# Kernel optimization log

Measured on AMD Instinct MI355X. Metric: run time of the kernel, lower is better.

The kernel has to match this reference:

```python
import jax, jax.numpy as jnp
import numpy as np
from jax import lax

SPATIAL = 4
DN = ('NCHW', 'OIHW', 'NCHW')

def setup_inputs() -> dict:
    key = jax.random.key(0)
    ks = jax.random.split(key, 6)
    b, c_in, h, w = 32, 256, 56, 56
    c_out, kk, n_exp, red = 256, 3, 3, 16
    fan = c_in * kk * kk
    return {
        'x': jax.random.normal(ks[0], (b, c_in, h, w), jnp.float32),
        'w_expert': jax.random.normal(ks[1], (n_exp, c_out, c_in, kk, kk), jnp.float32) / np.sqrt(fan),
        'route_conv_w': jax.random.normal(ks[2], (red, c_in), jnp.float32) / np.sqrt(c_in),
        'route_conv_b': jax.random.normal(ks[3], (red,), jnp.float32) * 0.05,
        'fc_w': jax.random.normal(ks[4], (n_exp, red * SPATIAL * SPATIAL), jnp.float32) / np.sqrt(red * SPATIAL * SPATIAL),
        'fc_b': jax.random.normal(ks[5], (n_exp,), jnp.float32) * 0.05,
    }

def _routing(x, route_conv_w, route_conv_b, fc_w, fc_b):
    b, c, h, w = x.shape
    # AdaptiveAvgPool2d(4): h, w divisible by 4 -> exact block mean
    pooled = x.reshape(b, c, SPATIAL, h // SPATIAL, SPATIAL, w // SPATIAL).mean(axis=(3, 5))  # [b,c,4,4]
    r = jnp.einsum('bcij,rc->brij', pooled, route_conv_w) + route_conv_b[None, :, None, None]
    r = jax.nn.relu(r).reshape(b, -1)                         # [b, red*16]
    r = jax.nn.relu(r @ fc_w.T + fc_b)                        # [b, n_exp]
    return jax.nn.sigmoid(r)

def reference(x, w_expert, route_conv_w, route_conv_b, fc_w, fc_b):
    rw = _routing(x, route_conv_w, route_conv_b, fc_w, fc_b)              # [b,k]
    cw = jnp.einsum('bk,koihw->boihw', rw, w_expert)                      # per-sample mixed weights
    def conv1(xi, wi):
        return lax.conv_general_dilated(xi[None], wi, window_strides=(1, 1),
                                        padding=[(1, 1), (1, 1)],
                                        dimension_numbers=DN)[0]
    return jax.vmap(conv1)(x, cw)  # [b, c_out, h, w]
```

## Files before the change

kernel.cpp:

```cpp
#include <hip/hip_runtime.h>
#include <hip/hip_bf16.h>
#include <stdint.h>

#define NB   32
#define CIN  256
#define COUT 256
#define WW   56
#define HW   3136
#define NEXP 3
#define KTOT 2304
#define XP   58
#define XPP  3364
#define NKT  36

typedef __attribute__((ext_vector_type(8))) __bf16 bf16x8;
typedef __attribute__((ext_vector_type(4))) float  f32x4;

#define OFF_RW     0
#define OFF_POOLED 1024
#define OFF_CWT    (1024 + 32*256*16*4)
#define CWT_BYTES  ((size_t)NB*COUT*KTOT*2)
#define OFF_XPAD   (OFF_CWT + CWT_BYTES)

#define PRE_XPAD 6272
#define PRE_POOL 8192
#define PRE_NBLK (PRE_XPAD + PRE_POOL + NB)

__global__ __launch_bounds__(256) void k_pre(const float* __restrict__ x,
                                             float* __restrict__ pooled,
                                             __bf16* __restrict__ xpad) {
    __shared__ __align__(16) char smem[8448];
    int blk = blockIdx.x;
    int t = threadIdx.x;

    if (blk < PRE_XPAD) {
        int pt = blk % 49;
        int r2 = blk / 49;
        int ct = r2 & 3;
        int b  = r2 >> 2;
        __bf16 (*lds)[66] = (__bf16(*)[66])smem;
        int pl = t & 63;
        int cb = t >> 6;
        const float* xb = x + ((size_t)(b * CIN + ct * 64)) * HW + pt * 64;
        #pragma unroll
        for (int ic = 0; ic < 16; ++ic) {
            int cl = ic * 4 + cb;
            lds[cl][pl] = (__bf16)xb[(size_t)cl * HW + pl];
        }
        __syncthreads();
        #pragma unroll
        for (int iw = 0; iw < 2; ++iw) {
            int idx = iw * 256 + t;
            int p_l = idx >> 3, c8 = (idx & 7) * 8;
            int p = pt * 64 + p_l;
            int y = p / WW, xx = p - y * WW;
            union { __bf16 h[8]; uint4 u; } pk;
            #pragma unroll
            for (int j = 0; j < 8; ++j) pk.h[j] = lds[c8 + j][p_l];
            __bf16* dst = xpad + ((size_t)b * XPP + (y + 1) * XP + (xx + 1)) * CIN
                          + ct * 64 + c8;
            *(uint4*)dst = pk.u;
        }
    } else if (blk < PRE_XPAD + PRE_POOL) {
        int j = blk - PRE_XPAD;
        int b = j >> 8, c = j & 255;
        float (*lds)[56] = (float(*)[56])smem;
        const float* xb = x + ((size_t)(b * CIN + c)) * HW;
        if (t < 224) {
            int xc = t % 56, yg = t / 56;
            const float* p = xb + (yg * 14) * WW + xc;
            float s = 0.f;
            #pragma unroll
            for (int r = 0; r < 14; ++r) s += p[r * WW];
            lds[yg][xc] = s;
        }
        __syncthreads();
        if (t < 16) {
            int sy = t >> 2, sx = t & 3;
            float s = 0.f;
            #pragma unroll
            for (int jj = 0; jj < 14; ++jj) s += lds[sy][sx * 14 + jj];
            pooled[(((size_t)b * CIN + c) << 4) + t] = s * (1.f / 196.f);
        }
    } else {
        int b = blk - (PRE_XPAD + PRE_POOL);
        for (int idx = t; idx < 228 * 32; idx += 256) {
            int pos = idx >> 5;
            int co = (idx & 31) * 8;
            int yy, xx;
            if (pos < 58)       { yy = 0;          xx = pos; }
            else if (pos < 116) { yy = 57;         xx = pos - 58; }
            else if (pos < 172) { yy = pos - 115;  xx = 0; }
            else                { yy = pos - 171;  xx = 57; }
            uint4 z = {0u, 0u, 0u, 0u};
            *(uint4*)(xpad + ((size_t)b * XPP + yy * XP + xx) * CIN + co) = z;
        }
    }
}

__global__ __launch_bounds__(256) void k_route(const float* __restrict__ pooled,
                                               const float* __restrict__ rcw,
                                               const float* __restrict__ rcb,
                                               const float* __restrict__ fcw,
                                               const float* __restrict__ fcb,
                                               float* __restrict__ rw) {
    int b = blockIdx.x;
    int t = threadIdx.x;
    int r = t >> 4, ij = t & 15;
    __shared__ float rbuf[256];
    const float* pb = pooled + (size_t)b * CIN * 16;
    float acc = rcb[r];
    for (int c = 0; c < CIN; ++c)
        acc += pb[c * 16 + ij] * rcw[r * CIN + c];
    rbuf[t] = fmaxf(acc, 0.f);
    __syncthreads();
    if (t < NEXP) {
        float a = fcb[t];
        for (int f = 0; f < 256; ++f) a += rbuf[f] * fcw[t * 256 + f];
        a = fmaxf(a, 0.f);
        rw[b * NEXP + t] = 1.f / (1.f + expf(-a));
    }
}

__global__ __launch_bounds__(256) void k_mixw(const float* __restrict__ we,
                                              const float* __restrict__ rw,
                                              __bf16* __restrict__ cwt) {
    int o = blockIdx.x;
    int i = threadIdx.x;
    float wv[3][9];
    #pragma unroll
    for (int e = 0; e < 3; ++e) {
        const float* p = we + (((size_t)e * COUT + o) * CIN + i) * 9;
        #pragma unroll
        for (int k = 0; k < 9; ++k) wv[e][k] = p[k];
    }
    for (int b = 0; b < NB; ++b) {
        float r0 = rw[b * 3 + 0], r1 = rw[b * 3 + 1], r2 = rw[b * 3 + 2];
        __bf16* op = cwt + ((size_t)(b * COUT + o)) * KTOT + i;
        #pragma unroll
        for (int k = 0; k < 9; ++k) {
            float v = r0 * wv[0][k] + r1 * wv[1][k] + r2 * wv[2][k];
            op[k * 256] = (__bf16)v;
        }
    }
}

#define GL16(g, l) __builtin_amdgcn_global_load_lds( \
    (const __attribute__((address_space(1))) uint32_t*)(g), \
    (__attribute__((address_space(3))) uint32_t*)(l), 16, 0, 0)

#define STAGE_A(o, kh, aoffn) do { \
    GL16(gA0 + (aoffn) + (kh)*64, LDS + (o)*32768 + (kh)*16384 + wid*1024); \
    GL16(gA1 + (aoffn) + (kh)*64, LDS + (o)*32768 + (kh)*16384 + 8192 + wid*1024); \
  } while (0)
#define STAGE_B(o, kh, boffn) do { \
    GL16(gB0 + (boffn) + (kh)*64, LDS + 65536 + (o)*32768 + (kh)*16384 + wid*1024); \
    GL16(gB1 + (boffn) + (kh)*64, LDS + 65536 + (o)*32768 + (kh)*16384 + 8192 + wid*1024); \
  } while (0)

#define BARRIER() do { \
    __builtin_amdgcn_sched_barrier(0); \
    __builtin_amdgcn_s_barrier(); \
    __builtin_amdgcn_sched_barrier(0); \
  } while (0)
#define VMCNT(n) do { \
    asm volatile("s_waitcnt vmcnt(" #n ")" ::: "memory"); \
    __builtin_amdgcn_sched_barrier(0); \
  } while (0)
#define LGKM0() do { \
    asm volatile("s_waitcnt lgkmcnt(0)" ::: "memory"); \
    __builtin_amdgcn_sched_barrier(0); \
  } while (0)

#define LOADF(F, base, kh, q) do { \
    F[0] = *(const bf16x8*)((base) + (kh)*16384 + (q)*4096 + 0); \
    F[1] = *(const bf16x8*)((base) + (kh)*16384 + (q)*4096 + 1024); \
    F[2] = *(const bf16x8*)((base) + (kh)*16384 + (q)*4096 + 2048); \
    F[3] = *(const bf16x8*)((base) + (kh)*16384 + (q)*4096 + 3072); \
  } while (0)
#define MM(qb, F) do { \
    _Pragma("unroll") \
    for (int mf = 0; mf < 4; ++mf) \
      _Pragma("unroll") \
      for (int nf = 0; nf < 4; ++nf) \
        acc[(qb) + mf][nf] = __builtin_amdgcn_mfma_f32_16x16x32_bf16( \
            F[mf], bq[nf], acc[(qb) + mf][nf], 0, 0, 0); \
  } while (0)

#define HALF(c, o, kh, aoffn, boffn) do { \
    VMCNT(4); \
    BARRIER(); \
    STAGE_A(o, kh, aoffn); \
    STAGE_B(o, kh, boffn); \
    { const char* aCur = LDS + (c) * 32768 + aRd; \
      const char* bCur = LDS + 65536 + (c) * 32768 + bRd; \
      LOADF(af, aCur, kh, 0); \
      LOADF(bq, bCur, kh, 0); \
      LOADF(ag, aCur, kh, 1); } \
    LGKM0(); \
    __builtin_amdgcn_s_setprio(1); \
    MM(0, af); \
    MM(4, ag); \
    __builtin_amdgcn_s_setprio(0); \
  } while (0)

__global__ __launch_bounds__(512, 2) void k_conv(const __bf16* __restrict__ cwt,
                                                 const __bf16* __restrict__ xpad,
                                                 float* __restrict__ out) {
    extern __shared__ __align__(16) char LDS[];

    int flat = blockIdx.x;
    int logical = (flat & 7) * 52 + (flat >> 3);
    int b  = logical / 13;
    int nt = logical - b * 13;

    int tid = threadIdx.x;
    int ln  = tid & 63;
    int wid = tid >> 6;
    int wr  = wid >> 2;
    int wc  = wid & 3;
    int fr  = ln & 15;
    int kw  = ln >> 4;
    int xsw = ((fr >> 1) & 3) << 4;

    const char *gA0, *gA1, *gB0, *gB1;
    {
        const char* cwb = (const char*)(cwt + (size_t)b * COUT * KTOT);
        const char* xpb = (const char*)(xpad + (size_t)b * XPP * CIN);
        #pragma unroll
        for (int i = 0; i < 2; ++i) {
            int L = i * 8192 + wid * 1024 + ln * 16;
            int U = L ^ (((L >> 7) & 3) << 4);
            int rowU = U >> 6;
            int kbU  = U & 63;
            const char* ga = cwb + (size_t)rowU * (KTOT * 2) + kbU;
            int p = nt * 256 + rowU; if (p > HW - 1) p = HW - 1;
            int y = p / WW, x = p - y * WW;
            const char* gb = xpb + (size_t)(y * XP + x) * (CIN * 2) + kbU;
            if (i == 0) { gA0 = ga; gB0 = gb; } else { gA1 = ga; gB1 = gb; }
        }
    }

    int aRd = (wr * 128 + fr) * 64 + ((kw * 16) ^ xsw);
    int bRd = (wc * 64 + fr) * 64 + ((kw * 16) ^ xsw);

    f32x4 acc[8][4];
    #pragma unroll
    for (int i = 0; i < 8; ++i)
        #pragma unroll
        for (int j = 0; j < 4; ++j)
            acc[i][j] = (f32x4){0.f, 0.f, 0.f, 0.f};

    bf16x8 af[4], ag[4], bq[4];

    STAGE_A(0, 0, 0);
    STAGE_B(0, 0, 0);
    STAGE_A(0, 1, 0);
    STAGE_B(0, 1, 0);

    for (int kt = 0; kt < NKT - 1; ++kt) {
        int c = kt & 1, o = c ^ 1;
        int ktn  = kt + 1;
        int aoffn = ktn * 128;
        int ktap = ktn >> 2;
        int kyn  = (ktap * 11) >> 5;
        int kxn  = ktap - kyn * 3;
        int boffn = (kyn * XP + kxn) * 512 + (ktn & 3) * 128;

        HALF(c, o, 0, aoffn, boffn);
        HALF(c, o, 1, aoffn, boffn);
    }

    {
        VMCNT(0);
        BARRIER();
        const char* aCur = LDS + 32768 + aRd;
        const char* bCur = LDS + 65536 + 32768 + bRd;
        LOADF(af, aCur, 0, 0); LOADF(bq, bCur, 0, 0); LOADF(ag, aCur, 0, 1);
        LGKM0();
        __builtin_amdgcn_s_setprio(1); MM(0, af); MM(4, ag);
        __builtin_amdgcn_s_setprio(0);
        LOADF(af, aCur, 1, 0); LOADF(bq, bCur, 1, 0); LOADF(ag, aCur, 1, 1);
        LGKM0();
        __builtin_amdgcn_s_setprio(1); MM(0, af); MM(4, ag);
        __builtin_amdgcn_s_setprio(0);
    }

    float* ob = out + ((size_t)(b * COUT + wr * 128)) * HW;
    int colbase = nt * 256 + wc * 64;
    int rb = (ln >> 4) * 4;
    #pragma unroll
    for (int q = 0; q < 2; ++q)
        #pragma unroll
        for (int nf = 0; nf < 4; ++nf) {
            int col = colbase + nf * 16 + fr;
            if (col < HW) {
                #pragma unroll
                for (int mf = 0; mf < 4; ++mf)
                    #pragma unroll
                    for (int r = 0; r < 4; ++r)
                        ob[(size_t)(q * 64 + mf * 16 + rb + r) * HW + col] =
                            acc[q * 4 + mf][nf][r];
            }
        }
}

extern "C" void kernel_launch(void* const* d_in, const int* in_sizes, int n_in,
                              void* d_out, int out_size, void* d_ws, size_t ws_size,
                              hipStream_t stream) {
    (void)in_sizes; (void)n_in; (void)out_size; (void)ws_size;
    const float* x   = (const float*)d_in[0];
    const float* we  = (const float*)d_in[1];
    const float* rcw = (const float*)d_in[2];
    const float* rcb = (const float*)d_in[3];
    const float* fcw = (const float*)d_in[4];
    const float* fcb = (const float*)d_in[5];
    float* out = (float*)d_out;

    char* ws = (char*)d_ws;
    float*  rw     = (float*)(ws + OFF_RW);
    float*  pooled = (float*)(ws + OFF_POOLED);
    __bf16* cwt    = (__bf16*)(ws + OFF_CWT);
    __bf16* xpad   = (__bf16*)(ws + OFF_XPAD);

    (void)hipFuncSetAttribute((const void*)k_conv,
                              hipFuncAttributeMaxDynamicSharedMemorySize, 131072);

    k_pre<<<PRE_NBLK, 256, 0, stream>>>(x, pooled, xpad);
    k_route<<<NB, 256, 0, stream>>>(pooled, rcw, rcb, fcw, fcb, rw);
    k_mixw<<<COUT, 256, 0, stream>>>(we, rw, cwt);
    k_conv<<<416, 512, 131072, stream>>>(cwt, xpad, out);
}
```

Baseline: 199.4 us.

## Use 4 waves with 128x128 per-wave tiles and early LDS fragment reads

```diff
diff --git a/kernel.cpp b/kernel.cpp
--- a/kernel.cpp
+++ b/kernel.cpp
@@ -150,12 +150,16 @@
     (__attribute__((address_space(3))) uint32_t*)(l), 16, 0, 0)
 
 #define STAGE_A(o, kh, aoffn) do { \
-    GL16(gA0 + (aoffn) + (kh)*64, LDS + (o)*32768 + (kh)*16384 + wid*1024); \
-    GL16(gA1 + (aoffn) + (kh)*64, LDS + (o)*32768 + (kh)*16384 + 8192 + wid*1024); \
+    GL16(gA0 + (aoffn) + (kh)*64, LDS + (o)*32768 + (kh)*16384 +     0 + wid*1024); \
+    GL16(gA1 + (aoffn) + (kh)*64, LDS + (o)*32768 + (kh)*16384 +  4096 + wid*1024); \
+    GL16(gA2 + (aoffn) + (kh)*64, LDS + (o)*32768 + (kh)*16384 +  8192 + wid*1024); \
+    GL16(gA3 + (aoffn) + (kh)*64, LDS + (o)*32768 + (kh)*16384 + 12288 + wid*1024); \
   } while (0)
 #define STAGE_B(o, kh, boffn) do { \
-    GL16(gB0 + (boffn) + (kh)*64, LDS + 65536 + (o)*32768 + (kh)*16384 + wid*1024); \
-    GL16(gB1 + (boffn) + (kh)*64, LDS + 65536 + (o)*32768 + (kh)*16384 + 8192 + wid*1024); \
+    GL16(gB0 + (boffn) + (kh)*64, LDS + 65536 + (o)*32768 + (kh)*16384 +     0 + wid*1024); \
+    GL16(gB1 + (boffn) + (kh)*64, LDS + 65536 + (o)*32768 + (kh)*16384 +  4096 + wid*1024); \
+    GL16(gB2 + (boffn) + (kh)*64, LDS + 65536 + (o)*32768 + (kh)*16384 +  8192 + wid*1024); \
+    GL16(gB3 + (boffn) + (kh)*64, LDS + 65536 + (o)*32768 + (kh)*16384 + 12288 + wid*1024); \
   } while (0)
 
 #define BARRIER() do { \
@@ -172,39 +176,41 @@
     __builtin_amdgcn_sched_barrier(0); \
   } while (0)
 
-#define LOADF(F, base, kh, q) do { \
-    F[0] = *(const bf16x8*)((base) + (kh)*16384 + (q)*4096 + 0); \
-    F[1] = *(const bf16x8*)((base) + (kh)*16384 + (q)*4096 + 1024); \
-    F[2] = *(const bf16x8*)((base) + (kh)*16384 + (q)*4096 + 2048); \
-    F[3] = *(const bf16x8*)((base) + (kh)*16384 + (q)*4096 + 3072); \
-  } while (0)
-#define MM(qb, F) do { \
+#define LOAD8(F, base) do { \
+    F[0] = *(const bf16x8*)((base) + 0); \
+    F[1] = *(const bf16x8*)((base) + 1024); \
+    F[2] = *(const bf16x8*)((base) + 2048); \
+    F[3] = *(const bf16x8*)((base) + 3072); \
+    F[4] = *(const bf16x8*)((base) + 4096); \
+    F[5] = *(const bf16x8*)((base) + 5120); \
+    F[6] = *(const bf16x8*)((base) + 6144); \
+    F[7] = *(const bf16x8*)((base) + 7168); \
+  } while (0)
+#define MMALL() do { \
+    __builtin_amdgcn_s_setprio(1); \
     _Pragma("unroll") \
-    for (int mf = 0; mf < 4; ++mf) \
+    for (int mf = 0; mf < 8; ++mf) \
       _Pragma("unroll") \
-      for (int nf = 0; nf < 4; ++nf) \
-        acc[(qb) + mf][nf] = __builtin_amdgcn_mfma_f32_16x16x32_bf16( \
-            F[mf], bq[nf], acc[(qb) + mf][nf], 0, 0, 0); \
+      for (int nf = 0; nf < 8; ++nf) \
+        acc[mf][nf] = __builtin_amdgcn_mfma_f32_16x16x32_bf16( \
+            af[mf], bq[nf], acc[mf][nf], 0, 0, 0); \
+    __builtin_amdgcn_s_setprio(0); \
   } while (0)
 
 #define HALF(c, o, kh, aoffn, boffn) do { \
-    VMCNT(4); \
+    VMCNT(8); \
     BARRIER(); \
+    { const char* aCur = LDS + (c)*32768 + (kh)*16384 + aRd; \
+      const char* bCur = LDS + 65536 + (c)*32768 + (kh)*16384 + bRd; \
+      LOAD8(af, aCur); \
+      LOAD8(bq, bCur); } \
     STAGE_A(o, kh, aoffn); \
     STAGE_B(o, kh, boffn); \
-    { const char* aCur = LDS + (c) * 32768 + aRd; \
-      const char* bCur = LDS + 65536 + (c) * 32768 + bRd; \
-      LOADF(af, aCur, kh, 0); \
-      LOADF(bq, bCur, kh, 0); \
-      LOADF(ag, aCur, kh, 1); } \
     LGKM0(); \
-    __builtin_amdgcn_s_setprio(1); \
-    MM(0, af); \
-    MM(4, ag); \
-    __builtin_amdgcn_s_setprio(0); \
-  } while (0)
-
-__global__ __launch_bounds__(512, 2) void k_conv(const __bf16* __restrict__ cwt,
+    MMALL(); \
+  } while (0)
+
+__global__ __launch_bounds__(256, 1) void k_conv(const __bf16* __restrict__ cwt,
                                                  const __bf16* __restrict__ xpad,
                                                  float* __restrict__ out) {
     extern __shared__ __align__(16) char LDS[];
@@ -217,19 +223,19 @@
     int tid = threadIdx.x;
     int ln  = tid & 63;
     int wid = tid >> 6;
-    int wr  = wid >> 2;
-    int wc  = wid & 3;
+    int wr  = wid >> 1;
+    int wc  = wid & 1;
     int fr  = ln & 15;
     int kw  = ln >> 4;
     int xsw = ((fr >> 1) & 3) << 4;
 
-    const char *gA0, *gA1, *gB0, *gB1;
+    const char *gA0, *gA1, *gA2, *gA3, *gB0, *gB1, *gB2, *gB3;
     {
         const char* cwb = (const char*)(cwt + (size_t)b * COUT * KTOT);
         const char* xpb = (const char*)(xpad + (size_t)b * XPP * CIN);
         #pragma unroll
-        for (int i = 0; i < 2; ++i) {
-            int L = i * 8192 + wid * 1024 + ln * 16;
+        for (int i = 0; i < 4; ++i) {
+            int L = i * 4096 + wid * 1024 + ln * 16;
             int U = L ^ (((L >> 7) & 3) << 4);
             int rowU = U >> 6;
             int kbU  = U & 63;
@@ -237,21 +243,24 @@
             int p = nt * 256 + rowU; if (p > HW - 1) p = HW - 1;
             int y = p / WW, x = p - y * WW;
             const char* gb = xpb + (size_t)(y * XP + x) * (CIN * 2) + kbU;
-            if (i == 0) { gA0 = ga; gB0 = gb; } else { gA1 = ga; gB1 = gb; }
+            if (i == 0)      { gA0 = ga; gB0 = gb; }
+            else if (i == 1) { gA1 = ga; gB1 = gb; }
+            else if (i == 2) { gA2 = ga; gB2 = gb; }
+            else             { gA3 = ga; gB3 = gb; }
         }
     }
 
     int aRd = (wr * 128 + fr) * 64 + ((kw * 16) ^ xsw);
-    int bRd = (wc * 64 + fr) * 64 + ((kw * 16) ^ xsw);
-
-    f32x4 acc[8][4];
+    int bRd = (wc * 128 + fr) * 64 + ((kw * 16) ^ xsw);
+
+    f32x4 acc[8][8];
     #pragma unroll
     for (int i = 0; i < 8; ++i)
         #pragma unroll
-        for (int j = 0; j < 4; ++j)
+        for (int j = 0; j < 8; ++j)
             acc[i][j] = (f32x4){0.f, 0.f, 0.f, 0.f};
 
-    bf16x8 af[4], ag[4], bq[4];
+    bf16x8 af[8], bq[8];
 
     STAGE_A(0, 0, 0);
     STAGE_B(0, 0, 0);
@@ -276,33 +285,29 @@
         BARRIER();
         const char* aCur = LDS + 32768 + aRd;
         const char* bCur = LDS + 65536 + 32768 + bRd;
-        LOADF(af, aCur, 0, 0); LOADF(bq, bCur, 0, 0); LOADF(ag, aCur, 0, 1);
+        LOAD8(af, aCur); LOAD8(bq, bCur);
         LGKM0();
-        __builtin_amdgcn_s_setprio(1); MM(0, af); MM(4, ag);
-        __builtin_amdgcn_s_setprio(0);
-        LOADF(af, aCur, 1, 0); LOADF(bq, bCur, 1, 0); LOADF(ag, aCur, 1, 1);
+        MMALL();
+        aCur += 16384; bCur += 16384;
+        LOAD8(af, aCur); LOAD8(bq, bCur);
         LGKM0();
-        __builtin_amdgcn_s_setprio(1); MM(0, af); MM(4, ag);
-        __builtin_amdgcn_s_setprio(0);
+        MMALL();
     }
 
     float* ob = out + ((size_t)(b * COUT + wr * 128)) * HW;
-    int colbase = nt * 256 + wc * 64;
+    int colbase = nt * 256 + wc * 128;
     int rb = (ln >> 4) * 4;
     #pragma unroll
-    for (int q = 0; q < 2; ++q)
-        #pragma unroll
-        for (int nf = 0; nf < 4; ++nf) {
-            int col = colbase + nf * 16 + fr;
-            if (col < HW) {
+    for (int nf = 0; nf < 8; ++nf) {
+        int col = colbase + nf * 16 + fr;
+        if (col < HW) {
+            #pragma unroll
+            for (int mf = 0; mf < 8; ++mf)
                 #pragma unroll
-                for (int mf = 0; mf < 4; ++mf)
-                    #pragma unroll
-                    for (int r = 0; r < 4; ++r)
-                        ob[(size_t)(q * 64 + mf * 16 + rb + r) * HW + col] =
-                            acc[q * 4 + mf][nf][r];
-            }
-        }
+                for (int r = 0; r < 4; ++r)
+                    ob[(size_t)(mf * 16 + rb + r) * HW + col] = acc[mf][nf][r];
+        }
+    }
 }
 
 extern "C" void kernel_launch(void* const* d_in, const int* in_sizes, int n_in,
@@ -329,5 +334,5 @@
     k_pre<<<PRE_NBLK, 256, 0, stream>>>(x, pooled, xpad);
     k_route<<<NB, 256, 0, stream>>>(pooled, rcw, rcb, fcw, fcb, rw);
     k_mixw<<<COUT, 256, 0, stream>>>(we, rw, cwt);
-    k_conv<<<416, 512, 131072, stream>>>(cwt, xpad, out);
-}
+    k_conv<<<416, 256, 131072, stream>>>(cwt, xpad, out);
+}
```

After: 204.4 us. 2.5% more time.

## Double-buffer LDS fragment reads in registers to overlap with MFMA

Applied to the files above, without the earlier changes.

```diff
diff --git a/kernel.cpp b/kernel.cpp
--- a/kernel.cpp
+++ b/kernel.cpp
@@ -158,49 +158,47 @@
     GL16(gB1 + (boffn) + (kh)*64, LDS + 65536 + (o)*32768 + (kh)*16384 + 8192 + wid*1024); \
   } while (0)
 
-#define BARRIER() do { \
-    __builtin_amdgcn_sched_barrier(0); \
-    __builtin_amdgcn_s_barrier(); \
-    __builtin_amdgcn_sched_barrier(0); \
-  } while (0)
+#define SB0() __builtin_amdgcn_sched_barrier(0)
+#define BARRIER() do { SB0(); __builtin_amdgcn_s_barrier(); SB0(); } while (0)
 #define VMCNT(n) do { \
-    asm volatile("s_waitcnt vmcnt(" #n ")" ::: "memory"); \
-    __builtin_amdgcn_sched_barrier(0); \
-  } while (0)
-#define LGKM0() do { \
-    asm volatile("s_waitcnt lgkmcnt(0)" ::: "memory"); \
-    __builtin_amdgcn_sched_barrier(0); \
-  } while (0)
-
-#define LOADF(F, base, kh, q) do { \
-    F[0] = *(const bf16x8*)((base) + (kh)*16384 + (q)*4096 + 0); \
-    F[1] = *(const bf16x8*)((base) + (kh)*16384 + (q)*4096 + 1024); \
-    F[2] = *(const bf16x8*)((base) + (kh)*16384 + (q)*4096 + 2048); \
-    F[3] = *(const bf16x8*)((base) + (kh)*16384 + (q)*4096 + 3072); \
-  } while (0)
-#define MM(qb, F) do { \
+    asm volatile("s_waitcnt vmcnt(" #n ")" ::: "memory"); SB0(); \
+  } while (0)
+#define LGKM(n) do { \
+    asm volatile("s_waitcnt lgkmcnt(" #n ")" ::: "memory"); SB0(); \
+  } while (0)
+
+#define READ12(AF, AG, BQ, c, kh) do { \
+    const char* aCur = LDS + (c)*32768 + (kh)*16384 + aRd; \
+    const char* bCur = LDS + 65536 + (c)*32768 + (kh)*16384 + bRd; \
+    AF[0] = *(const bf16x8*)(aCur + 0); \
+    AF[1] = *(const bf16x8*)(aCur + 1024); \
+    AF[2] = *(const bf16x8*)(aCur + 2048); \
+    AF[3] = *(const bf16x8*)(aCur + 3072); \
+    BQ[0] = *(const bf16x8*)(bCur + 0); \
+    BQ[1] = *(const bf16x8*)(bCur + 1024); \
+    BQ[2] = *(const bf16x8*)(bCur + 2048); \
+    BQ[3] = *(const bf16x8*)(bCur + 3072); \
+    AG[0] = *(const bf16x8*)(aCur + 4096); \
+    AG[1] = *(const bf16x8*)(aCur + 5120); \
+    AG[2] = *(const bf16x8*)(aCur + 6144); \
+    AG[3] = *(const bf16x8*)(aCur + 7168); \
+    SB0(); \
+  } while (0)
+
+#define MM32(AF, AG, BQ) do { \
+    __builtin_amdgcn_s_setprio(1); \
     _Pragma("unroll") \
     for (int mf = 0; mf < 4; ++mf) \
       _Pragma("unroll") \
       for (int nf = 0; nf < 4; ++nf) \
-        acc[(qb) + mf][nf] = __builtin_amdgcn_mfma_f32_16x16x32_bf16( \
-            F[mf], bq[nf], acc[(qb) + mf][nf], 0, 0, 0); \
-  } while (0)
-
-#define HALF(c, o, kh, aoffn, boffn) do { \
-    VMCNT(4); \
-    BARRIER(); \
-    STAGE_A(o, kh, aoffn); \
-    STAGE_B(o, kh, boffn); \
-    { const char* aCur = LDS + (c) * 32768 + aRd; \
-      const char* bCur = LDS + 65536 + (c) * 32768 + bRd; \
-      LOADF(af, aCur, kh, 0); \
-      LOADF(bq, bCur, kh, 0); \
-      LOADF(ag, aCur, kh, 1); } \
-    LGKM0(); \
-    __builtin_amdgcn_s_setprio(1); \
-    MM(0, af); \
-    MM(4, ag); \
+        acc[mf][nf] = __builtin_amdgcn_mfma_f32_16x16x32_bf16( \
+            AF[mf], BQ[nf], acc[mf][nf], 0, 0, 0); \
+    _Pragma("unroll") \
+    for (int mf = 0; mf < 4; ++mf) \
+      _Pragma("unroll") \
+      for (int nf = 0; nf < 4; ++nf) \
+        acc[4 + mf][nf] = __builtin_amdgcn_mfma_f32_16x16x32_bf16( \
+            AG[mf], BQ[nf], acc[4 + mf][nf], 0, 0, 0); \
     __builtin_amdgcn_s_setprio(0); \
   } while (0)
 
@@ -251,39 +249,48 @@
         for (int j = 0; j < 4; ++j)
             acc[i][j] = (f32x4){0.f, 0.f, 0.f, 0.f};
 
-    bf16x8 af[4], ag[4], bq[4];
-
-    STAGE_A(0, 0, 0);
-    STAGE_B(0, 0, 0);
-    STAGE_A(0, 1, 0);
-    STAGE_B(0, 1, 0);
-
-    for (int kt = 0; kt < NKT - 1; ++kt) {
-        int c = kt & 1, o = c ^ 1;
-        int ktn  = kt + 1;
-        int aoffn = ktn * 128;
-        int ktap = ktn >> 2;
-        int kyn  = (ktap * 11) >> 5;
-        int kxn  = ktap - kyn * 3;
-        int boffn = (kyn * XP + kxn) * 512 + (ktn & 3) * 128;
-
-        HALF(c, o, 0, aoffn, boffn);
-        HALF(c, o, 1, aoffn, boffn);
+    bf16x8 afA[4], agA[4], bqA[4];
+    bf16x8 afB[4], agB[4], bqB[4];
+
+    STAGE_A(0, 0, 0);  STAGE_B(0, 0, 0);
+    STAGE_A(0, 1, 0);  STAGE_B(0, 1, 0);
+    STAGE_A(1, 0, 128); STAGE_B(1, 0, 128);
+    VMCNT(8);
+    BARRIER();
+    READ12(afA, agA, bqA, 0, 0);
+
+    for (int T = 0; T < 35; ++T) {
+        int c = T & 1, o = c ^ 1;
+        int t1 = T + 1, t2 = T + 2;
+        int tap1 = t1 >> 2, ky1 = (tap1 * 11) >> 5, kx1 = tap1 - ky1 * 3;
+        int ao1 = t1 * 128;
+        int bo1 = (ky1 * XP + kx1) * 512 + (t1 & 3) * 128;
+        int tap2 = t2 >> 2, ky2 = (tap2 * 11) >> 5, kx2 = tap2 - ky2 * 3;
+        int ao2 = t2 * 128;
+        int bo2 = (ky2 * XP + kx2) * 512 + (t2 & 3) * 128;
+
+        VMCNT(4);
+        BARRIER();
+        READ12(afB, agB, bqB, c, 1);
+        STAGE_A(o, 1, ao1); STAGE_B(o, 1, bo1);
+        LGKM(12);
+        MM32(afA, agA, bqA);
+        VMCNT(4);
+        BARRIER();
+        READ12(afA, agA, bqA, o, 0);
+        if (T <= 33) { STAGE_A(c, 0, ao2); STAGE_B(c, 0, bo2); }
+        LGKM(12);
+        MM32(afB, agB, bqB);
     }
 
     {
         VMCNT(0);
         BARRIER();
-        const char* aCur = LDS + 32768 + aRd;
-        const char* bCur = LDS + 65536 + 32768 + bRd;
-        LOADF(af, aCur, 0, 0); LOADF(bq, bCur, 0, 0); LOADF(ag, aCur, 0, 1);
-        LGKM0();
-        __builtin_amdgcn_s_setprio(1); MM(0, af); MM(4, ag);
-        __builtin_amdgcn_s_setprio(0);
-        LOADF(af, aCur, 1, 0); LOADF(bq, bCur, 1, 0); LOADF(ag, aCur, 1, 1);
-        LGKM0();
-        __builtin_amdgcn_s_setprio(1); MM(0, af); MM(4, ag);
-        __builtin_amdgcn_s_setprio(0);
+        READ12(afB, agB, bqB, 1, 1);
+        LGKM(12);
+        MM32(afA, agA, bqA);
+        LGKM(0);
+        MM32(afB, agB, bqB);
     }
 
     float* ob = out + ((size_t)(b * COUT + wr * 128)) * HW;
```

New measurement: 197.4 us. About the same (-1.0%).
